# Performance work log

Hardware: AMD Instinct MI355X
Metric: run time of the kernel (lower is better)

Reference implementation:

```python
import jax, jax.numpy as jnp
import numpy as np

N_NODES = 100000


def _gcn_norm(edge_index, num_nodes):
    # PyG gcn_norm with add_self_loops=True, edge_weight=1:
    # A_hat = A + I; norm_e = deg^{-1/2}[src] * deg^{-1/2}[dst]
    loop = jnp.arange(num_nodes, dtype=edge_index.dtype)
    src = jnp.concatenate([edge_index[0], loop])
    dst = jnp.concatenate([edge_index[1], loop])
    deg = jax.ops.segment_sum(jnp.ones_like(src, dtype=jnp.float32), dst,
                              num_segments=num_nodes)
    dinv = jnp.where(deg > 0, jax.lax.rsqrt(deg), 0.0)
    norm = dinv[src] * dinv[dst]  # [E + N]
    return src, dst, norm


def _gcn_conv(x, src, dst, norm, W, b, num_nodes):
    h = x @ W                                  # [N, out] dense GEMM
    msg = h[src] * norm[:, None]               # gather + scale per edge
    out = jax.ops.segment_sum(msg, dst, num_segments=num_nodes)
    return out + b


def setup_inputs() -> dict:
    key = jax.random.key(0)
    k1, k2, k3, k4, k5, k6 = jax.random.split(key, 6)
    in_c, hid_c, out_c = 128, 128, 64
    E = 3200000
    x = jax.random.normal(k1, (N_NODES, in_c), dtype=jnp.float32)
    edge_index = jax.random.randint(k2, (2, E), 0, N_NODES, dtype=jnp.int64)
    # Glorot-style init for GCNConv linear weights, zero bias (PyG default)
    W1 = jax.random.normal(k3, (in_c, hid_c), dtype=jnp.float32) / np.sqrt(in_c)
    b1 = jnp.zeros((hid_c,), dtype=jnp.float32)
    W2 = jax.random.normal(k4, (hid_c, out_c), dtype=jnp.float32) / np.sqrt(hid_c)
    b2 = jnp.zeros((out_c,), dtype=jnp.float32)
    return {"x": x, "edge_index": edge_index, "W1": W1, "b1": b1,
            "W2": W2, "b2": b2}


def reference(x, edge_index, W1, b1, W2, b2):
    # Dropout is identity in eval mode (F.dropout(training=False)).
    src, dst, norm = _gcn_norm(edge_index, N_NODES)
    h = _gcn_conv(x, src, dst, norm, W1, b1, N_NODES)
    out = _gcn_conv(h, src, dst, norm, W2, b2, N_NODES)
    return out
```

## Files before the change

### kernel.cpp

```cpp
#include <hip/hip_runtime.h>
#include <hip/hip_fp16.h>
#include <cstdint>
#include <cstddef>


#define NB    391
#define BSH   8
#define CAPS  32
#define PBLK  512
#define OVCAP 4096
#define CAPB  9216

typedef _Float16 half8 __attribute__((ext_vector_type(8)));
typedef float    floatx4 __attribute__((ext_vector_type(4)));


__global__ __launch_bounds__(256) void partition_k(
    const int* __restrict__ src, const int* __restrict__ dst,
    int* __restrict__ ovcur, unsigned* __restrict__ ovrecs,
    unsigned* __restrict__ tailbuf, int* __restrict__ tailcnt, int E) {
    __shared__ unsigned stag[NB][CAPS + 1];
    __shared__ int scnt[NB];
    const int t = threadIdx.x;
    for (int i = t; i < NB; i += 256) scnt[i] = 0;
    __syncthreads();

    const int Q = E >> 2;
    const int per = (Q + PBLK - 1) / PBLK;
    const int qbeg = blockIdx.x * per;
    const int qend = min(qbeg + per, Q);
    const int4* src4 = (const int4*)src;
    const int4* dst4 = (const int4*)dst;

    for (int q = qbeg + t; q < qend; q += 256) {
        const int4 s4 = src4[q];
        const int4 d4 = dst4[q];
#pragma unroll
        for (int j = 0; j < 4; ++j) {
            const int s = (&s4.x)[j], d = (&d4.x)[j];
            const int b = d >> BSH;
            const unsigned rec = ((unsigned)(d & 255) << 17) | (unsigned)s;
            const int slot = atomicAdd(&scnt[b], 1);
            if (slot < CAPS) stag[b][slot] = rec;
            else { const int p = atomicAdd(&ovcur[b], 1); ovrecs[(size_t)b * OVCAP + p] = rec; }
        }
    }
    if (blockIdx.x == 0) {
        for (int e = (E & ~3) + t; e < E; e += 256) {
            const int s = src[e], d = dst[e];
            const int b = d >> BSH;
            const unsigned rec = ((unsigned)(d & 255) << 17) | (unsigned)s;
            const int slot = atomicAdd(&scnt[b], 1);
            if (slot < CAPS) stag[b][slot] = rec;
            else { const int p = atomicAdd(&ovcur[b], 1); ovrecs[(size_t)b * OVCAP + p] = rec; }
        }
    }
    __syncthreads();

    for (int i = t; i < NB * CAPS; i += 256) {
        const int b = i >> 5, j = i & 31;
        if (j < min(scnt[b], CAPS))
            tailbuf[((size_t)b * PBLK + blockIdx.x) * CAPS + j] = stag[b][j];
    }
    for (int b = t; b < NB; b += 256)
        tailcnt[blockIdx.x * NB + b] = min(scnt[b], CAPS);
}

__global__ __launch_bounds__(256) void build_k(
    const unsigned* __restrict__ ovrecs, const int* __restrict__ ovcur,
    const unsigned* __restrict__ tailbuf, const int* __restrict__ tailcnt,
    int* __restrict__ rbeg, int* __restrict__ rend,
    int* __restrict__ csr, float* __restrict__ dinv, int N) {
    __shared__ int tcs[PBLK];
    __shared__ int soff[PBLK];
    __shared__ int sseg[256];
    __shared__ unsigned lrec[CAPB];
    __shared__ int cnt[256];
    __shared__ int scan[256];
    __shared__ int lpos[256];
    __shared__ int tcum_sh;
    const int t = threadIdx.x, b = blockIdx.x;
    const int n0 = b << BSH;
    const int nn = min(256, N - n0);
    const int gbase = b * CAPB;
    const size_t tb0 = (size_t)b * PBLK * CAPS;
    const int ov = ovcur[b];

    for (int i = t; i < PBLK; i += 256) tcs[i] = tailcnt[i * NB + b];
    cnt[t] = 0;
    __syncthreads();

    const int a0 = tcs[2 * t], a1 = tcs[2 * t + 1];
    sseg[t] = a0 + a1;
    __syncthreads();
    for (int o = 1; o < 256; o <<= 1) {
        int x = (t >= o) ? sseg[t - o] : 0;
        __syncthreads(); sseg[t] += x; __syncthreads();
    }
    const int ex2 = sseg[t] - (a0 + a1);
    soff[2 * t] = ex2;
    soff[2 * t + 1] = ex2 + a0;
    if (t == 255) tcum_sh = sseg[255];
    __syncthreads();
    const int tcum = tcum_sh;

    for (int i = t; i < PBLK * CAPS; i += 256) {
        const int seg = i >> 5, j = i & 31;
        if (j < tcs[seg]) lrec[soff[seg] + j] = tailbuf[tb0 + i];
    }
    for (int i = t; i < ov; i += 256) lrec[tcum + i] = ovrecs[(size_t)b * OVCAP + i];
    __syncthreads();

    const int tot = tcum + ov;
    for (int i = t; i < tot; i += 256) atomicAdd(&cnt[lrec[i] >> 17], 1);
    __syncthreads();

    scan[t] = cnt[t];
    __syncthreads();
    for (int o = 1; o < 256; o <<= 1) {
        int x = (t >= o) ? scan[t - o] : 0;
        __syncthreads(); scan[t] += x; __syncthreads();
    }
    const int excl = scan[t] - cnt[t];
    lpos[t] = excl;
    if (t < nn) {
        rbeg[n0 + t] = gbase + excl;
        rend[n0 + t] = gbase + scan[t];
        dinv[n0 + t] = rsqrtf((float)(cnt[t] + 1));
    }
    __syncthreads();

    for (int i = t; i < tot; i += 256) {
        const unsigned r = lrec[i];
        const int pq = atomicAdd(&lpos[r >> 17], 1);
        csr[gbase + pq] = (int)(r & 0x1FFFFu);
    }
}

__global__ __launch_bounds__(256) void w12_k(
    const float* __restrict__ W1, const float* __restrict__ W2,
    const float* __restrict__ b1, _Float16* __restrict__ BhiT,
    _Float16* __restrict__ BloT, float* __restrict__ c2) {
    const int t = threadIdx.x;
    if (blockIdx.x < 32) {
        const int r = blockIdx.x * 4 + (t >> 6);
        const int c = t & 63;
        float acc = 0.f;
        for (int k = 0; k < 128; ++k) acc += W1[r * 128 + k] * W2[k * 64 + c];
        const _Float16 h = (_Float16)acc;
        BhiT[c * 128 + r] = h;
        BloT[c * 128 + r] = (_Float16)(acc - (float)h);
    } else if (t < 64) {
        float acc = 0.f;
        for (int k = 0; k < 128; ++k) acc += b1[k] * W2[k * 64 + t];
        c2[t] = acc;
    }
}

__global__ __launch_bounds__(256) void gemm_mfma_k(
    const float* __restrict__ X, const _Float16* __restrict__ BhiT,
    const _Float16* __restrict__ BloT, const float* __restrict__ dinv,
    __half* __restrict__ g, int N) {
    const int t = threadIdx.x;
    const int wave = t >> 6, lane = t & 63;
    const int m16 = lane & 15;
    const int quad = lane >> 4;
    const int rowbase = blockIdx.x * 64 + wave * 16;
    const int arow = min(rowbase + m16, N - 1);

    floatx4 acc[4] = {{0.f,0.f,0.f,0.f},{0.f,0.f,0.f,0.f},
                      {0.f,0.f,0.f,0.f},{0.f,0.f,0.f,0.f}};

#pragma unroll
    for (int ks = 0; ks < 4; ++ks) {
        const int k0 = ks * 32 + quad * 8;
        const float4 xa = *(const float4*)(X + (size_t)arow * 128 + k0);
        const float4 xb = *(const float4*)(X + (size_t)arow * 128 + k0 + 4);
        const float xs[8] = {xa.x, xa.y, xa.z, xa.w, xb.x, xb.y, xb.z, xb.w};
        half8 ahi, alo;
#pragma unroll
        for (int j = 0; j < 8; ++j) {
            const _Float16 h = (_Float16)xs[j];
            ahi[j] = h;
            alo[j] = (_Float16)(xs[j] - (float)h);
        }
#pragma unroll
        for (int c = 0; c < 4; ++c) {
            const int n = c * 16 + m16;
            const half8 bhi = *(const half8*)(BhiT + n * 128 + k0);
            const half8 blo = *(const half8*)(BloT + n * 128 + k0);
            acc[c] = __builtin_amdgcn_mfma_f32_16x16x32_f16(ahi, bhi, acc[c], 0, 0, 0);
            acc[c] = __builtin_amdgcn_mfma_f32_16x16x32_f16(ahi, blo, acc[c], 0, 0, 0);
            acc[c] = __builtin_amdgcn_mfma_f32_16x16x32_f16(alo, bhi, acc[c], 0, 0, 0);
        }
    }

#pragma unroll
    for (int r = 0; r < 4; ++r) {
        const int grow = rowbase + quad * 4 + r;
        if (grow < N) {
            const float di = dinv[grow];
#pragma unroll
            for (int c = 0; c < 4; ++c)
                g[(size_t)grow * 64 + c * 16 + m16] = __float2half(acc[c][r] * di);
        }
    }
}

template <int PASS2>
__global__ __launch_bounds__(256) void agg_k(
    const __half* __restrict__ gin, const int* __restrict__ rbeg,
    const int* __restrict__ rend, const int* __restrict__ csr,
    const float* __restrict__ dinv, void* __restrict__ outp,
    float* __restrict__ p, const float* __restrict__ c2,
    const float* __restrict__ b2, int N) {
    const int d = (blockIdx.x * 256 + threadIdx.x) >> 6;
    const int lane = threadIdx.x & 63;
    if (d >= N) return;
    const int pair = lane & 31;
    const int sub  = lane >> 5;
    const int beg = rbeg[d], end = rend[d];
    const int mid = beg + ((end - beg + 1) >> 1);
    const float di = dinv[d];
    const __half2* g2 = (const __half2*)gin;

    const float2 fself = __half22float2(g2[((size_t)d << 5) + pair]);

    float accx = 0.f, accy = 0.f;
    float accp = (!PASS2 && sub == 0) ? di : 0.f;

    int e        = sub ? mid : beg;
    const int eE = sub ? end : mid;

    for (; e + 8 <= eE; e += 8) {
        int s[8];
#pragma unroll
        for (int j = 0; j < 8; ++j) s[j] = csr[e + j];
        float2 f[8];
#pragma unroll
        for (int j = 0; j < 8; ++j) f[j] = __half22float2(g2[((size_t)s[j] << 5) + pair]);
        if (!PASS2) {
#pragma unroll
            for (int j = 0; j < 8; ++j) accp += dinv[s[j]];
        }
#pragma unroll
        for (int j = 0; j < 8; ++j) { accx += f[j].x; accy += f[j].y; }
    }
    if (e + 4 <= eE) {
        int s[4];
#pragma unroll
        for (int j = 0; j < 4; ++j) s[j] = csr[e + j];
        float2 f[4];
#pragma unroll
        for (int j = 0; j < 4; ++j) f[j] = __half22float2(g2[((size_t)s[j] << 5) + pair]);
        if (!PASS2) {
#pragma unroll
            for (int j = 0; j < 4; ++j) accp += dinv[s[j]];
        }
#pragma unroll
        for (int j = 0; j < 4; ++j) { accx += f[j].x; accy += f[j].y; }
        e += 4;
    }
    for (; e < eE; ++e) {
        const int s = csr[e];
        const float2 f = __half22float2(g2[((size_t)s << 5) + pair]);
        if (!PASS2) accp += dinv[s];
        accx += f.x; accy += f.y;
    }

    accx += __shfl(accx, pair + 32);
    accy += __shfl(accy, pair + 32);
    if (!PASS2) accp += __shfl(accp, pair + 32);

    if (sub == 0) {
        accx += fself.x; accy += fself.y;
        if (PASS2) {
            const float2 cc = ((const float2*)c2)[pair];
            const float2 bb = ((const float2*)b2)[pair];
            const float pd = p[d];
            float2 o;
            o.x = accx * di + pd * cc.x + bb.x;
            o.y = accy * di + pd * cc.y + bb.y;
            ((float2*)outp)[((size_t)d << 5) + pair] = o;
        } else {
            const float sc = di * di;
            ((__half2*)outp)[((size_t)d << 5) + pair] =
                __floats2half2_rn(accx * sc, accy * sc);
            if (lane == 0) p[d] = di * accp;
        }
    }
}

extern "C" void kernel_launch(void* const* d_in, const int* in_sizes, int n_in,
                              void* d_out, int out_size, void* d_ws, size_t ws_size,
                              hipStream_t stream) {
    const float* x  = (const float*)d_in[0];
    const int*   ei = (const int*)d_in[1];
    const float* W1 = (const float*)d_in[2];
    const float* b1 = (const float*)d_in[3];
    const float* W2 = (const float*)d_in[4];
    const float* b2 = (const float*)d_in[5];
    float* out = (float*)d_out;

    const int N = in_sizes[0] / 128;
    const int E = in_sizes[1] / 2;
    const int* src = ei;
    const int* dst = ei + E;

    char* ws = (char*)d_ws;
    auto take = [&](size_t bytes) { char* q = ws; ws += (bytes + 255) & ~(size_t)255; return q; };
    int*      ovcur   = (int*)     take(NB * 4);
    int*      rbeg    = (int*)     take((size_t)N * 4);
    int*      rendp   = (int*)     take((size_t)N * 4);
    float*    dinv    = (float*)   take((size_t)N * 4);
    float*    pbuf    = (float*)   take((size_t)N * 4);
    _Float16* BhiT    = (_Float16*)take(128 * 64 * 2);
    _Float16* BloT    = (_Float16*)take(128 * 64 * 2);
    float*    c2      = (float*)   take(64 * 4);
    int*      tailcnt = (int*)     take((size_t)NB * PBLK * 4);
    unsigned* ovrecs  = (unsigned*)take((size_t)NB * OVCAP * 4);
    unsigned* tailbuf = (unsigned*)take((size_t)NB * PBLK * CAPS * 4);
    int*      csr     = (int*)     take((size_t)NB * CAPB * 4);
    __half*   g       = (__half*)  take((size_t)N * 64 * 2);
    __half*   t1      = (__half*)  take((size_t)N * 64 * 2);

    hipMemsetAsync(ovcur, 0, NB * 4, stream);

    partition_k<<<PBLK, 256, 0, stream>>>(src, dst, ovcur, ovrecs, tailbuf, tailcnt, E);
    build_k<<<NB, 256, 0, stream>>>(ovrecs, ovcur, tailbuf, tailcnt, rbeg, rendp, csr, dinv, N);
    w12_k<<<33, 256, 0, stream>>>(W1, W2, b1, BhiT, BloT, c2);
    gemm_mfma_k<<<(N + 63) / 64, 256, 0, stream>>>(x, BhiT, BloT, dinv, g, N);

    const int aggBlocks = (int)(((size_t)N * 64 + 255) / 256);
    agg_k<0><<<aggBlocks, 256, 0, stream>>>(g,  rbeg, rendp, csr, dinv, t1,  pbuf, c2, b2, N);
    agg_k<1><<<aggBlocks, 256, 0, stream>>>(t1, rbeg, rendp, csr, dinv, out, pbuf, c2, b2, N);
}
```

Baseline: 327.9 us.

## Use 16-byte half8 gathers with 8 edges in flight per wavefront in aggregation

```diff
diff --git a/kernel.cpp b/kernel.cpp
--- a/kernel.cpp
+++ b/kernel.cpp
@@ -217,75 +217,86 @@
     const int d = (blockIdx.x * 256 + threadIdx.x) >> 6;
     const int lane = threadIdx.x & 63;
     if (d >= N) return;
-    const int pair = lane & 31;
-    const int sub  = lane >> 5;
+    const int w    = lane & 7;
+    const int slot = lane >> 3;
     const int beg = rbeg[d], end = rend[d];
-    const int mid = beg + ((end - beg + 1) >> 1);
     const float di = dinv[d];
-    const __half2* g2 = (const __half2*)gin;
-
-    const float2 fself = __half22float2(g2[((size_t)d << 5) + pair]);
-
-    float accx = 0.f, accy = 0.f;
-    float accp = (!PASS2 && sub == 0) ? di : 0.f;
-
-    int e        = sub ? mid : beg;
-    const int eE = sub ? end : mid;
-
-    for (; e + 8 <= eE; e += 8) {
-        int s[8];
-#pragma unroll
-        for (int j = 0; j < 8; ++j) s[j] = csr[e + j];
-        float2 f[8];
-#pragma unroll
-        for (int j = 0; j < 8; ++j) f[j] = __half22float2(g2[((size_t)s[j] << 5) + pair]);
-        if (!PASS2) {
-#pragma unroll
-            for (int j = 0; j < 8; ++j) accp += dinv[s[j]];
-        }
-#pragma unroll
-        for (int j = 0; j < 8; ++j) { accx += f[j].x; accy += f[j].y; }
-    }
-    if (e + 4 <= eE) {
-        int s[4];
-#pragma unroll
-        for (int j = 0; j < 4; ++j) s[j] = csr[e + j];
-        float2 f[4];
-#pragma unroll
-        for (int j = 0; j < 4; ++j) f[j] = __half22float2(g2[((size_t)s[j] << 5) + pair]);
-        if (!PASS2) {
-#pragma unroll
-            for (int j = 0; j < 4; ++j) accp += dinv[s[j]];
-        }
-#pragma unroll
-        for (int j = 0; j < 4; ++j) { accx += f[j].x; accy += f[j].y; }
-        e += 4;
-    }
-    for (; e < eE; ++e) {
-        const int s = csr[e];
-        const float2 f = __half22float2(g2[((size_t)s << 5) + pair]);
-        if (!PASS2) accp += dinv[s];
-        accx += f.x; accy += f.y;
-    }
-
-    accx += __shfl(accx, pair + 32);
-    accy += __shfl(accy, pair + 32);
-    if (!PASS2) accp += __shfl(accp, pair + 32);
-
-    if (sub == 0) {
-        accx += fself.x; accy += fself.y;
+    const half8* __restrict__ grow = (const half8*)gin;
+
+    const half8 vself = grow[((size_t)d << 3) + w];
+
+    float acc[8];
+#pragma unroll
+    for (int q = 0; q < 8; ++q) acc[q] = 0.f;
+    float accp = (!PASS2 && slot == 0) ? di : 0.f;
+
+    auto accum = [&](half8 f) {
+        const __half2* h2 = (const __half2*)&f;
+#pragma unroll
+        for (int q = 0; q < 4; ++q) {
+            const float2 t2 = __half22float2(h2[q]);
+            acc[2 * q]     += t2.x;
+            acc[2 * q + 1] += t2.y;
+        }
+    };
+
+    int e = beg + slot;
+    while (e + 24 < end) {
+        const int s0 = csr[e], s1 = csr[e + 8], s2 = csr[e + 16], s3 = csr[e + 24];
+        const half8 f0 = grow[((size_t)s0 << 3) + w];
+        const half8 f1 = grow[((size_t)s1 << 3) + w];
+        const half8 f2 = grow[((size_t)s2 << 3) + w];
+        const half8 f3 = grow[((size_t)s3 << 3) + w];
+        if (!PASS2) accp += dinv[s0] + dinv[s1] + dinv[s2] + dinv[s3];
+        accum(f0); accum(f1); accum(f2); accum(f3);
+        e += 32;
+    }
+    if (e + 8 < end) {
+        const int s0 = csr[e], s1 = csr[e + 8];
+        const half8 f0 = grow[((size_t)s0 << 3) + w];
+        const half8 f1 = grow[((size_t)s1 << 3) + w];
+        if (!PASS2) accp += dinv[s0] + dinv[s1];
+        accum(f0); accum(f1);
+        e += 16;
+    }
+    while (e < end) {
+        const int s0 = csr[e];
+        const half8 f0 = grow[((size_t)s0 << 3) + w];
+        if (!PASS2) accp += dinv[s0];
+        accum(f0);
+        e += 8;
+    }
+
+#pragma unroll
+    for (int m = 8; m <= 32; m <<= 1) {
+#pragma unroll
+        for (int q = 0; q < 8; ++q) acc[q] += __shfl_xor(acc[q], m);
+        if (!PASS2) accp += __shfl_xor(accp, m);
+    }
+
+    if (slot == 0) {
+        const __half2* sh2 = (const __half2*)&vself;
+#pragma unroll
+        for (int q = 0; q < 4; ++q) {
+            const float2 t2 = __half22float2(sh2[q]);
+            acc[2 * q]     += t2.x;
+            acc[2 * q + 1] += t2.y;
+        }
         if (PASS2) {
-            const float2 cc = ((const float2*)c2)[pair];
-            const float2 bb = ((const float2*)b2)[pair];
             const float pd = p[d];
-            float2 o;
-            o.x = accx * di + pd * cc.x + bb.x;
-            o.y = accy * di + pd * cc.y + bb.y;
-            ((float2*)outp)[((size_t)d << 5) + pair] = o;
+            float o[8];
+#pragma unroll
+            for (int q = 0; q < 8; ++q)
+                o[q] = acc[q] * di + pd * c2[w * 8 + q] + b2[w * 8 + q];
+            float4* op = (float4*)outp + ((size_t)d << 4) + w * 2;
+            op[0] = make_float4(o[0], o[1], o[2], o[3]);
+            op[1] = make_float4(o[4], o[5], o[6], o[7]);
         } else {
             const float sc = di * di;
-            ((__half2*)outp)[((size_t)d << 5) + pair] =
-                __floats2half2_rn(accx * sc, accy * sc);
+            half8 ov;
+#pragma unroll
+            for (int q = 0; q < 8; ++q) ov[q] = (_Float16)(acc[q] * sc);
+            ((half8*)outp)[((size_t)d << 3) + w] = ov;
             if (lane == 0) p[d] = di * accp;
         }
     }
```

Measured after the change: 314.2 us. 4.2% less time.
